# Optimization experiments

Measured on AMD Instinct MI355X. Metric: run time of the kernel, lower is better.

Reference implementation:

```python
import jax, jax.numpy as jnp
import numpy as np

B, T, C, N = 2, 2048, 4096, 4096

def setup_inputs() -> dict:
    key = jax.random.key(0)
    k1, k2, k3, k4 = jax.random.split(key, 4)
    y = jax.random.normal(k1, (B, T, C), dtype=jnp.float32)
    # quantized weight: uint8 codes in [0,255], stored/used as float after upcast
    weight = jnp.round(jax.random.uniform(k2, (C, N), dtype=jnp.float32) * 255.0)
    rng = jax.random.uniform(k3, (1, 1, C), dtype=jnp.float32) * 0.01  # per-input-channel scale
    offset = jax.random.normal(k4, (C,), dtype=jnp.float32) * 0.01    # per-input-channel offset
    return {"y": y, "weight": weight, "rng": rng, "offset": offset}

def reference(y, weight, rng, offset):
    # yv = y.reshape(-1,C) @ offset -> [B,T,1] correction term
    yv = jnp.einsum('btc,c->bt', y, offset)[..., None]
    # (y * range) @ weight  (dequantized GEMM) + correction
    out = jnp.einsum('btc,cn->btn', y * rng, weight) + yv
    return out
```

## Files before the change

kernel.cpp:

```cpp
#include <hip/hip_runtime.h>

typedef unsigned short u16;
typedef unsigned int u32;
typedef unsigned char u8;
typedef signed char i8;

typedef int i32x4 __attribute__((ext_vector_type(4)));

__device__ inline void gld16(const i8* g, i8* l) {
    __builtin_amdgcn_global_load_lds((const __attribute__((address_space(1))) void*)g,
                                     (__attribute__((address_space(3))) void*)l,
                                     16, 0, 0);
}

__global__ __launch_bounds__(256) void prep_kernel(const float* __restrict__ y,
                                                   const float* __restrict__ rng,
                                                   const float* __restrict__ off,
                                                   const float* __restrict__ w,
                                                   uint4* __restrict__ qy,
                                                   uint4* __restrict__ wq,
                                                   float* __restrict__ sp,
                                                   float* __restrict__ tv) {
    __shared__ i8 tile[64][68];
    __shared__ float ra[4], rs1[4], rs2[4];
    const int tid = threadIdx.x;

    if (blockIdx.x < 4096) {
        const int row = blockIdx.x;
        const float* yr = y + (size_t)row * 4096;
        const int base = tid * 16;

        float ysr[16];
        float amax = 0.0f, s1 = 0.0f, s2 = 0.0f;
        #pragma unroll
        for (int ii = 0; ii < 4; ++ii) {
            float4 v = *(const float4*)&yr[base + ii * 4];
            float4 g = *(const float4*)&rng[base + ii * 4];
            float4 o = *(const float4*)&off[base + ii * 4];
            float p0 = v.x * g.x, p1 = v.y * g.y, p2 = v.z * g.z, p3 = v.w * g.w;
            ysr[ii * 4 + 0] = p0; ysr[ii * 4 + 1] = p1;
            ysr[ii * 4 + 2] = p2; ysr[ii * 4 + 3] = p3;
            s1 += p0 + p1 + p2 + p3;
            s2 += v.x * o.x + v.y * o.y + v.z * o.z + v.w * o.w;
            amax = fmaxf(amax, fmaxf(fmaxf(fabsf(p0), fabsf(p1)), fmaxf(fabsf(p2), fabsf(p3))));
        }
        #pragma unroll
        for (int d = 32; d > 0; d >>= 1) {
            amax = fmaxf(amax, __shfl_down(amax, d));
            s1 += __shfl_down(s1, d);
            s2 += __shfl_down(s2, d);
        }
        const int wv = tid >> 6;
        if ((tid & 63) == 0) { ra[wv] = amax; rs1[wv] = s1; rs2[wv] = s2; }
        __syncthreads();
        const float sm = fmaxf(fmaxf(ra[0], ra[1]), fmaxf(ra[2], ra[3]));
        const float inv = sm > 0.0f ? 127.0f / sm : 0.0f;

        u32 d[4];
        #pragma unroll
        for (int g = 0; g < 4; ++g) {
            u32 b0 = (u8)(i8)(int)rintf(ysr[g * 4 + 0] * inv);
            u32 b1 = (u8)(i8)(int)rintf(ysr[g * 4 + 1] * inv);
            u32 b2 = (u8)(i8)(int)rintf(ysr[g * 4 + 2] * inv);
            u32 b3 = (u8)(i8)(int)rintf(ysr[g * 4 + 3] * inv);
            d[g] = b0 | (b1 << 8) | (b2 << 16) | (b3 << 24);
        }
        const int j = (tid & 7) ^ (row & 7);
        qy[(size_t)row * 256 + (tid >> 3) * 8 + j] = make_uint4(d[0], d[1], d[2], d[3]);
        if (tid == 0) {
            sp[row] = sm / 127.0f;
            tv[row] = 128.0f * (rs1[0] + rs1[1] + rs1[2] + rs1[3])
                            + (rs2[0] + rs2[1] + rs2[2] + rs2[3]);
        }
    } else {
        const int bid = blockIdx.x - 4096;
        const int n0 = (bid & 63) * 64;
        const int k0 = (bid >> 6) * 64;
        const int c4 = tid & 15;
        const int r0 = tid >> 4;
        #pragma unroll
        for (int i = 0; i < 4; ++i) {
            int kk = r0 + i * 16;
            float4 v = *(const float4*)&w[(size_t)(k0 + kk) * 4096 + n0 + c4 * 4];
            u32 b0 = (u8)(i8)((int)v.x - 128);
            u32 b1 = (u8)(i8)((int)v.y - 128);
            u32 b2 = (u8)(i8)((int)v.z - 128);
            u32 b3 = (u8)(i8)((int)v.w - 128);
            *(u32*)&tile[kk][c4 * 4] = b0 | (b1 << 8) | (b2 << 16) | (b3 << 24);
        }
        __syncthreads();
        const int nl = tid >> 2;
        const int ci = tid & 3;
        const int l = ((k0 >> 4) & 7) + ci;
        const int j = l ^ ((n0 + nl) & 7);
        u32 d[4];
        #pragma unroll
        for (int g = 0; g < 4; ++g) {
            int kl = ci * 16 + g * 4;
            d[g] = (u32)(u8)tile[kl + 0][nl] | ((u32)(u8)tile[kl + 1][nl] << 8)
                 | ((u32)(u8)tile[kl + 2][nl] << 16) | ((u32)(u8)tile[kl + 3][nl] << 24);
        }
        wq[(size_t)(n0 + nl) * 256 + (k0 >> 7) * 8 + j] = make_uint4(d[0], d[1], d[2], d[3]);
    }
}

__global__ __launch_bounds__(512, 2) void gemm_kernel(const i8* __restrict__ qy,
                                                      const i8* __restrict__ wq,
                                                      const float* __restrict__ sp,
                                                      const float* __restrict__ tv,
                                                      float* __restrict__ out) {
    __shared__ i8 As[2][256 * 128];
    __shared__ i8 Bs[2][256 * 128];

    const int bid = blockIdx.x;
    const int xcd = bid & 7;
    const int jj = bid >> 3;
    const int bn = (xcd * 2 + (jj & 1)) * 256;
    const int bm = (jj >> 1) * 256;

    const int tid = (int)threadIdx.x;
    const int lane = tid & 63;
    const int wv = tid >> 6;
    const int wm = (wv >> 2) * 128;
    const int wn = (wv & 3) * 64;
    const int r = lane & 15;
    const int q = lane >> 4;
    const int col0 = (q ^ (r & 7)) << 4;

    const int offA0 = (wm + r) * 128 + col0;
    const int offB0 = (wn + r) * 128 + col0;
    const int offA1 = offA0 ^ 64;
    const int offB1 = offB0 ^ 64;

    const int rsub = lane >> 3;
    const int jsub = lane & 7;
    const i8* aP0 = qy + (size_t)(bm + wv * 8 + rsub) * 4096 + jsub * 16;
    const i8* bP0 = wq + (size_t)(bn + (wv >> 2) * 64 + (wv & 3) * 8 + rsub) * 4096 + jsub * 16;
    const int lAo = wv * 1024 + lane * 16;
    const int lBo = (wv >> 2) * 8192 + (wv & 3) * 1024 + lane * 16;

    size_t koff = 0;

#define STAGE_A(WB, H) do {                                                   \
        gld16(aP0 + koff + (size_t)((H) * 64) * 4096,       &As[WB][lAo + (H) * 8192]);          \
        gld16(aP0 + koff + (size_t)((H) * 64 + 128) * 4096, &As[WB][lAo + (H) * 8192 + 16384]);  \
    } while (0)
#define STAGE_B(WB, H) do {                                                   \
        gld16(bP0 + koff + (size_t)((H) * 32) * 4096,       &Bs[WB][lBo + (H) * 4096]);          \
        gld16(bP0 + koff + (size_t)((H) * 32 + 128) * 4096, &Bs[WB][lBo + (H) * 4096 + 16384]);  \
    } while (0)

    i32x4 acc[8][4] = {};
    i32x4 a[4][2], aa[4][2], b[4][2];

    STAGE_A(0, 0); STAGE_B(0, 0); STAGE_B(0, 1);
    __builtin_amdgcn_sched_barrier(0);
    STAGE_A(0, 1);
    koff = 128;
    asm volatile("s_waitcnt vmcnt(2)" ::: "memory");
    __builtin_amdgcn_s_barrier();

#define RD_A4K(RB, MB, DST, KS)                                               \
    _Pragma("unroll")                                                         \
    for (int mi = 0; mi < 4; ++mi) {                                          \
        DST[mi][KS] = *(const i32x4*)&As[RB][((KS) ? offA1 : offA0) + (MB + mi) * 2048]; \
    }
#define RD_B4K(RB, KS)                                                        \
    _Pragma("unroll")                                                         \
    for (int ni = 0; ni < 4; ++ni) {                                          \
        b[ni][KS] = *(const i32x4*)&Bs[RB][((KS) ? offB1 : offB0) + ni * 2048]; \
    }
#define MM16(MB, SRC, KS)                                                     \
    _Pragma("unroll")                                                         \
    for (int mi = 0; mi < 4; ++mi) {                                          \
        _Pragma("unroll")                                                     \
        for (int ni = 0; ni < 4; ++ni) {                                      \
            acc[MB + mi][ni] = __builtin_amdgcn_mfma_i32_16x16x64_i8(         \
                SRC[mi][KS], b[ni][KS], acc[MB + mi][ni], 0, 0, 0);           \
        }                                                                     \
    }

#define KTILE(RB, WB, PF)                                                     \
    do {                                                                      \
                           \
        RD_A4K(RB, 0, a, 0);                                                  \
        RD_B4K(RB, 0);                      \
        RD_A4K(RB, 0, a, 1);                                                  \
        RD_B4K(RB, 1);                                \
        if (PF) { STAGE_A(WB, 0); STAGE_B(WB, 0); }                           \
        __builtin_amdgcn_s_setprio(1);                                        \
        asm volatile("s_waitcnt lgkmcnt(8)" ::: "memory");    \
        __builtin_amdgcn_sched_barrier(0);                                    \
        MM16(0, a, 0);                    \
        asm volatile("s_waitcnt lgkmcnt(0)" ::: "memory");                    \
        __builtin_amdgcn_sched_barrier(0);                                    \
        MM16(0, a, 1);                                                        \
        __builtin_amdgcn_s_setprio(0);                                        \
        if (PF) asm volatile("s_waitcnt vmcnt(4)" ::: "memory");   \
        else    asm volatile("s_waitcnt vmcnt(0)" ::: "memory");              \
        __builtin_amdgcn_s_barrier();                                         \
                              \
        RD_A4K(RB, 4, aa, 0);                                                 \
        RD_A4K(RB, 4, aa, 1);                                                 \
        if (PF) { STAGE_B(WB, 1); __builtin_amdgcn_sched_barrier(0); STAGE_A(WB, 1); } \
        __builtin_amdgcn_s_setprio(1);                                        \
        asm volatile("s_waitcnt lgkmcnt(4)" ::: "memory");   \
        __builtin_amdgcn_sched_barrier(0);                                    \
        MM16(4, aa, 0);                            \
        asm volatile("s_waitcnt lgkmcnt(0)" ::: "memory");                    \
        __builtin_amdgcn_sched_barrier(0);                                    \
        MM16(4, aa, 1);                                                       \
        __builtin_amdgcn_s_setprio(0);                                        \
        if (PF) asm volatile("s_waitcnt vmcnt(2)" ::: "memory");   \
        else    asm volatile("s_waitcnt vmcnt(0)" ::: "memory");              \
        __builtin_amdgcn_s_barrier();                                         \
        koff += 128;                                                          \
    } while (0)

    #pragma unroll 1
    for (int t = 0; t < 15; ++t) {
        KTILE(0, 1, 1);
        KTILE(1, 0, 1);
    }
    KTILE(0, 1, 1);
    KTILE(1, 0, 0);

#undef KTILE
#undef MM16
#undef RD_B4K
#undef RD_A4K
#undef STAGE_B
#undef STAGE_A

    #pragma unroll
    for (int mi = 0; mi < 8; ++mi) {
        #pragma unroll
        for (int rr = 0; rr < 4; ++rr) {
            const int gm = bm + wm + mi * 16 + q * 4 + rr;
            const float sc = sp[gm];
            const float tt = tv[gm];
            #pragma unroll
            for (int ni = 0; ni < 4; ++ni) {
                const int gn = bn + wn + ni * 16 + r;
                out[(size_t)gm * 4096 + gn] = sc * (float)acc[mi][ni][rr] + tt;
            }
        }
    }
}

extern "C" void kernel_launch(void* const* d_in, const int* in_sizes, int n_in,
                              void* d_out, int out_size, void* d_ws, size_t ws_size,
                              hipStream_t stream) {
    const float* y   = (const float*)d_in[0];
    const float* w   = (const float*)d_in[1];
    const float* rng = (const float*)d_in[2];
    const float* off = (const float*)d_in[3];
    float* out = (float*)d_out;

    i8* qy = (i8*)d_ws;
    i8* wq = qy + (size_t)4096 * 4096;
    float* sp = (float*)(wq + (size_t)4096 * 4096);
    float* tv = sp + 4096;

    prep_kernel<<<8192, 256, 0, stream>>>(y, rng, off, w, (uint4*)qy, (uint4*)wq, sp, tv);
    gemm_kernel<<<256, 512, 0, stream>>>(qy, wq, sp, tv, out);
}
```

Before: 235.1 us.

## Restructure int8 GEMM k-tile to a single barrier with all prefetch issued upfront

Replaces the two-phase k-tile, which used a mid-tile barrier and split prefetch halves, with one phase per k-tile. All four global-to-LDS prefetch loads are issued at the start, and the second half's LDS reads are interleaved with the MFMA groups under finer lgkmcnt waits. This removes one workgroup barrier per k-tile and lets the second-half LDS reads overlap the first-half MFMAs. In exchange, each tile ends with a full vmcnt(0) wait, so global load latency must now be hidden within a single tile's compute.

```diff
diff --git a/kernel.cpp b/kernel.cpp
--- a/kernel.cpp
+++ b/kernel.cpp
@@ -153,12 +153,12 @@
     i32x4 acc[8][4] = {};
     i32x4 a[4][2], aa[4][2], b[4][2];
 
-    STAGE_A(0, 0); STAGE_B(0, 0); STAGE_B(0, 1);
-    __builtin_amdgcn_sched_barrier(0);
-    STAGE_A(0, 1);
+    STAGE_A(0, 0); STAGE_B(0, 0); STAGE_B(0, 1); STAGE_A(0, 1);
     koff = 128;
-    asm volatile("s_waitcnt vmcnt(2)" ::: "memory");
+    asm volatile("s_waitcnt vmcnt(0)" ::: "memory");
     __builtin_amdgcn_s_barrier();
+
+#define SB __builtin_amdgcn_sched_barrier(0)
 
 #define RD_A4K(RB, MB, DST, KS)                                               \
     _Pragma("unroll")                                                         \
@@ -182,37 +182,27 @@
 
 #define KTILE(RB, WB, PF)                                                     \
     do {                                                                      \
-                           \
-        RD_A4K(RB, 0, a, 0);                                                  \
-        RD_B4K(RB, 0);                      \
-        RD_A4K(RB, 0, a, 1);                                                  \
-        RD_B4K(RB, 1);                                \
-        if (PF) { STAGE_A(WB, 0); STAGE_B(WB, 0); }                           \
+                                            \
+        RD_A4K(RB, 0, a, 0); RD_B4K(RB, 0); SB;                               \
+                                            \
+        RD_A4K(RB, 0, a, 1); RD_B4K(RB, 1); SB;                               \
+          \
+        if (PF) { STAGE_A(WB, 0); STAGE_B(WB, 0); STAGE_B(WB, 1); STAGE_A(WB, 1); } \
+        SB;                                                                   \
         __builtin_amdgcn_s_setprio(1);                                        \
-        asm volatile("s_waitcnt lgkmcnt(8)" ::: "memory");    \
-        __builtin_amdgcn_sched_barrier(0);                                    \
-        MM16(0, a, 0);                    \
-        asm volatile("s_waitcnt lgkmcnt(0)" ::: "memory");                    \
-        __builtin_amdgcn_sched_barrier(0);                                    \
-        MM16(0, a, 1);                                                        \
-        __builtin_amdgcn_s_setprio(0);                                        \
-        if (PF) asm volatile("s_waitcnt vmcnt(4)" ::: "memory");   \
-        else    asm volatile("s_waitcnt vmcnt(0)" ::: "memory");              \
-        __builtin_amdgcn_s_barrier();                                         \
-                              \
-        RD_A4K(RB, 4, aa, 0);                                                 \
-        RD_A4K(RB, 4, aa, 1);                                                 \
-        if (PF) { STAGE_B(WB, 1); __builtin_amdgcn_sched_barrier(0); STAGE_A(WB, 1); } \
-        __builtin_amdgcn_s_setprio(1);                                        \
-        asm volatile("s_waitcnt lgkmcnt(4)" ::: "memory");   \
-        __builtin_amdgcn_sched_barrier(0);                                    \
-        MM16(4, aa, 0);                            \
-        asm volatile("s_waitcnt lgkmcnt(0)" ::: "memory");                    \
-        __builtin_amdgcn_sched_barrier(0);                                    \
+        asm volatile("s_waitcnt lgkmcnt(8)" ::: "memory"); SB;   \
+        MM16(0, a, 0); SB;                                                    \
+                        \
+        RD_A4K(RB, 4, aa, 0); SB;                                             \
+        RD_A4K(RB, 4, aa, 1); SB;                                             \
+        asm volatile("s_waitcnt lgkmcnt(8)" ::: "memory"); SB;   \
+        MM16(0, a, 1); SB;                                                    \
+        asm volatile("s_waitcnt lgkmcnt(4)" ::: "memory"); SB;   \
+        MM16(4, aa, 0); SB;                                                   \
+        asm volatile("s_waitcnt lgkmcnt(0)" ::: "memory"); SB;   \
         MM16(4, aa, 1);                                                       \
         __builtin_amdgcn_s_setprio(0);                                        \
-        if (PF) asm volatile("s_waitcnt vmcnt(2)" ::: "memory");   \
-        else    asm volatile("s_waitcnt vmcnt(0)" ::: "memory");              \
+        asm volatile("s_waitcnt vmcnt(0)" ::: "memory");                      \
         __builtin_amdgcn_s_barrier();                                         \
         koff += 128;                                                          \
     } while (0)
@@ -229,6 +219,7 @@
 #undef MM16
 #undef RD_B4K
 #undef RD_A4K
+#undef SB
 #undef STAGE_B
 #undef STAGE_A
 
```

After: 230.5 us. 2.0% less time.
